# Kernel tuning notes

Measured on AMD Instinct MI355X. Metric: run time of the kernel, lower is better.

The kernel has to match this reference:

```python
import jax, jax.numpy as jnp
import numpy as np

S, E, H, D, F = 2048, 1280, 16, 80, 5120
EPS = 1e-6


def _ln(x, g, b):
    m = x.mean(-1, keepdims=True)
    v = x.var(-1, keepdims=True)
    return (x - m) * jax.lax.rsqrt(v + EPS) * g + b


def _rotate_half(x):
    x1, x2 = jnp.split(x, 2, axis=-1)
    return jnp.concatenate([-x2, x1], axis=-1)


def _quick_gelu(x):
    return x * jax.nn.sigmoid(1.702 * x)


def setup_inputs() -> dict:
    key = jax.random.key(0)
    ks = jax.random.split(key, 12)
    inp = {
        "hidden_states": jax.random.normal(ks[0], (S, E), jnp.float32),
        "attention_mask": jnp.ones((1, 1, S, S), jnp.bool_),
        "cos": jax.random.uniform(ks[1], (S, D), jnp.float32),
        "sin": jax.random.uniform(ks[2], (S, D), jnp.float32),
        "ln1_g": jnp.ones((E,), jnp.float32),
        "ln1_b": jnp.zeros((E,), jnp.float32),
        "ln2_g": jnp.ones((E,), jnp.float32),
        "ln2_b": jnp.zeros((E,), jnp.float32),
        "w_qkv": jax.random.normal(ks[3], (E, 3 * E), jnp.float32) * (E ** -0.5),
        "b_qkv": jax.random.normal(ks[4], (3 * E,), jnp.float32) * 0.02,
        "w_o": jax.random.normal(ks[5], (E, E), jnp.float32) * (E ** -0.5),
        "b_o": jax.random.normal(ks[6], (E,), jnp.float32) * 0.02,
        "w_fc1": jax.random.normal(ks[7], (E, F), jnp.float32) * (E ** -0.5),
        "b_fc1": jax.random.normal(ks[8], (F,), jnp.float32) * 0.02,
        "w_fc2": jax.random.normal(ks[9], (F, E), jnp.float32) * (F ** -0.5),
        "b_fc2": jax.random.normal(ks[10], (E,), jnp.float32) * 0.02,
    }
    return inp


def reference(hidden_states, attention_mask, cos, sin, ln1_g, ln1_b, ln2_g, ln2_b,
              w_qkv, b_qkv, w_o, b_o, w_fc1, b_fc1, w_fc2, b_fc2):
    x = hidden_states  # [S, E]
    h = _ln(x, ln1_g, ln1_b)
    qkv = h @ w_qkv + b_qkv  # [S, 3E]
    q, k, v = jnp.split(qkv, 3, axis=-1)
    q = q.reshape(S, H, D)
    k = k.reshape(S, H, D)
    v = v.reshape(S, H, D)
    # rotary in fp32, cos/sin broadcast over head axis: [S, 1, D]
    c = cos[:, None, :].astype(jnp.float32)
    s = sin[:, None, :].astype(jnp.float32)
    qf, kf = q.astype(jnp.float32), k.astype(jnp.float32)
    q = (qf * c + _rotate_half(qf) * s).astype(q.dtype)
    k = (kf * c + _rotate_half(kf) * s).astype(k.dtype)
    # attention scores [H, S, S]
    scores = jnp.einsum('shd,thd->hst', q, k) / np.float32(np.sqrt(D))
    scores = jnp.where(attention_mask[0], scores, jnp.finfo(scores.dtype).min)
    probs = jax.nn.softmax(scores.astype(jnp.float32), axis=-1).astype(q.dtype)
    attn = jnp.einsum('hst,thd->shd', probs, v).reshape(S, E)
    attn = attn @ w_o + b_o
    x = x + attn
    h2 = _ln(x, ln2_g, ln2_b)
    mlp = _quick_gelu(h2 @ w_fc1 + b_fc1) @ w_fc2 + b_fc2
    return x + mlp
```

## Files before the change

### kernel.cpp

```cpp
#include <hip/hip_runtime.h>
#include <stdint.h>
#include <math.h>

#define S_LEN 2048
#define EMB   1280
#define NHEAD 16
#define HDIM  80
#define FDIM  5120

typedef __bf16 bf16x8 __attribute__((ext_vector_type(8)));
typedef float  f32x4  __attribute__((ext_vector_type(4)));
typedef int    i32x4  __attribute__((ext_vector_type(4)));
typedef unsigned short u16x8 __attribute__((ext_vector_type(8)));
typedef unsigned short u16x4 __attribute__((ext_vector_type(4)));

__device__ __forceinline__ float b2f(unsigned short u) {
    union { float f; unsigned int i; } x; x.i = ((unsigned int)u) << 16; return x.f;
}
__device__ __forceinline__ unsigned short f2b(float f) {
    union { float f; unsigned int i; } x; x.f = f;
    unsigned int r = x.i + 0x7FFFu + ((x.i >> 16) & 1u);
    return (unsigned short)(r >> 16);
}

__device__ __forceinline__ float wave_rsum(float v) {
    #pragma unroll
    for (int o = 32; o; o >>= 1) v += __shfl_down(v, o);
    return v;
}

__device__ __forceinline__ void trans64(
    const float* __restrict__ in, unsigned short* __restrict__ out,
    int R, int C, int bx, int by, int tid)
{
    __shared__ unsigned short tile[64][65];
    int c0 = bx * 64, r0 = by * 64;
    int tx = tid & 63, ty = tid >> 6;
    #pragma unroll
    for (int j = 0; j < 16; ++j) {
        int row = ty + j * 4;
        tile[row][tx] = f2b(in[(size_t)(r0 + row) * C + c0 + tx]);
    }
    __syncthreads();
    #pragma unroll
    for (int j = 0; j < 16; ++j) {
        int row = ty + j * 4;
        out[(size_t)(c0 + row) * R + r0 + tx] = tile[tx][row];
    }
}

__global__ __launch_bounds__(256) void transpose4_kernel(
    const float* __restrict__ w_qkv, unsigned short* __restrict__ wT_qkv,
    const float* __restrict__ w_o,   unsigned short* __restrict__ wT_o,
    const float* __restrict__ w_fc1, unsigned short* __restrict__ wT_fc1,
    const float* __restrict__ w_fc2, unsigned short* __restrict__ wT_fc2)
{
    int id = blockIdx.x, tid = threadIdx.x;
    if (id < 1200) {
        trans64(w_qkv, wT_qkv, 1280, 3840, id % 60, id / 60, tid);
    } else if (id < 1600) {
        int t = id - 1200;
        trans64(w_o, wT_o, 1280, 1280, t % 20, t / 20, tid);
    } else if (id < 3200) {
        int t = id - 1600;
        trans64(w_fc1, wT_fc1, 1280, 5120, t % 80, t / 80, tid);
    } else {
        int t = id - 3200;
        trans64(w_fc2, wT_fc2, 5120, 1280, t % 20, t / 20, tid);
    }
}

__global__ __launch_bounds__(256) void ln_kernel(
    const float* __restrict__ x,
    const float* __restrict__ g,
    const float* __restrict__ b,
    unsigned short* __restrict__ out)
{
    int row = blockIdx.x, tid = threadIdx.x;
    int lane = tid & 63, wave = tid >> 6;
    const float* xr = x + (size_t)row * EMB;
    float v[5], s = 0.f, ss = 0.f;
    #pragma unroll
    for (int i = 0; i < 5; ++i) {
        float f = xr[tid + i * 256];
        v[i] = f; s += f; ss += f * f;
    }
    s = wave_rsum(s); ss = wave_rsum(ss);
    __shared__ float rs[4], rss[4];
    if (lane == 0) { rs[wave] = s; rss[wave] = ss; }
    __syncthreads();
    float st  = rs[0] + rs[1] + rs[2] + rs[3];
    float sst = rss[0] + rss[1] + rss[2] + rss[3];
    float mean = st * (1.0f / EMB);
    float var  = sst * (1.0f / EMB) - mean * mean;
    float inv  = rsqrtf(var + 1e-6f);
    unsigned short* orow = out + (size_t)row * EMB;
    #pragma unroll
    for (int i = 0; i < 5; ++i) {
        int c = tid + i * 256;
        orow[c] = f2b((v[i] - mean) * inv * g[c] + b[c]);
    }
}

template<int EPI, int OM, int SPLIT>
__global__ __launch_bounds__(256) void gemm_kernel(
    const unsigned short* __restrict__ A,
    const unsigned short* __restrict__ Bt,
    const float* __restrict__ bias,
    const float* __restrict__ res,
    void* __restrict__ Cv,
    int M, int N, int K)
{
    __shared__ __align__(16) unsigned short As[2][128 * 32];
    __shared__ __align__(16) unsigned short Bs[2][128 * 32];

    int tid = threadIdx.x;
    int lane = tid & 63, wave = tid >> 6;
    int m0 = blockIdx.x * 128, n0 = blockIdx.y * 128;
    int wm = (wave >> 1) * 64, wn = (wave & 1) * 64;
    int kc = K / SPLIT;
    int kbeg = blockIdx.z * kc;
    const int NITER = kc / 32;

    f32x4 acc[4][4];
    #pragma unroll
    for (int i = 0; i < 4; ++i)
        #pragma unroll
        for (int j = 0; j < 4; ++j)
            acc[i][j] = (f32x4){0.f, 0.f, 0.f, 0.f};

    const unsigned short* Ap0 = A  + (size_t)(m0 + (tid >> 2)) * K + (tid & 3) * 8 + kbeg;
    const unsigned short* Ap1 = Ap0 + (size_t)64 * K;
    const unsigned short* Bp0 = Bt + (size_t)(n0 + (tid >> 2)) * K + (tid & 3) * 8 + kbeg;
    const unsigned short* Bp1 = Bp0 + (size_t)64 * K;

    int arow = lane & 15, aq = (lane >> 4) * 8;
    int aoff[4], boff[4];
    #pragma unroll
    for (int i = 0; i < 4; ++i) {
        aoff[i] = (wm + i * 16 + arow) * 32 + aq;
        boff[i] = (wn + i * 16 + arow) * 32 + aq;
    }

    i32x4 rA0a, rA1a, rB0a, rB1a, rA0b, rA1b, rB0b, rB1b;

    rA0b = *(const i32x4*)(Ap0);
    rA1b = *(const i32x4*)(Ap1);
    rB0b = *(const i32x4*)(Bp0);
    rB1b = *(const i32x4*)(Bp1);
    *(i32x4*)&As[0][tid * 8]        = rA0b;
    *(i32x4*)&As[0][2048 + tid * 8] = rA1b;
    *(i32x4*)&Bs[0][tid * 8]        = rB0b;
    *(i32x4*)&Bs[0][2048 + tid * 8] = rB1b;
    if (NITER > 1) {
        rA0a = *(const i32x4*)(Ap0 + 32);
        rA1a = *(const i32x4*)(Ap1 + 32);
        rB0a = *(const i32x4*)(Bp0 + 32);
        rB1a = *(const i32x4*)(Bp1 + 32);
    }
    __syncthreads();

#define GSTEP(IT, AW0, AW1, BW0, BW1, AL0, AL1, BL0, BL1)                    \
    {                                                                         \
        const int cur = (IT) & 1, nb = cur ^ 1;                               \
        if ((IT) + 1 < NITER) {                                               \
            *(i32x4*)&As[nb][tid * 8]        = AW0;                           \
            *(i32x4*)&As[nb][2048 + tid * 8] = AW1;                           \
            *(i32x4*)&Bs[nb][tid * 8]        = BW0;                           \
            *(i32x4*)&Bs[nb][2048 + tid * 8] = BW1;                           \
        }                                                                     \
        if ((IT) + 2 < NITER) {                                               \
            int ko = ((IT) + 2) * 32;                                         \
            AL0 = *(const i32x4*)(Ap0 + ko);                                  \
            AL1 = *(const i32x4*)(Ap1 + ko);                                  \
            BL0 = *(const i32x4*)(Bp0 + ko);                                  \
            BL1 = *(const i32x4*)(Bp1 + ko);                                  \
        }                                                                     \
        bf16x8 af[4], bfm[4];                                                 \
        _Pragma("unroll") for (int i = 0; i < 4; ++i) {                       \
            af[i]  = *(const bf16x8*)&As[cur][aoff[i]];                       \
            bfm[i] = *(const bf16x8*)&Bs[cur][boff[i]];                       \
        }                                                                     \
        _Pragma("unroll") for (int mi = 0; mi < 4; ++mi)                      \
            _Pragma("unroll") for (int ni = 0; ni < 4; ++ni)                  \
                acc[mi][ni] = __builtin_amdgcn_mfma_f32_16x16x32_bf16(        \
                    af[mi], bfm[ni], acc[mi][ni], 0, 0, 0);                   \
        __syncthreads();                                                      \
    }

    for (int it = 0; it < NITER; it += 2) {
        GSTEP(it,     rA0a, rA1a, rB0a, rB1a, rA0b, rA1b, rB0b, rB1b)
        GSTEP(it + 1, rA0b, rA1b, rB0b, rB1b, rA0a, rA1a, rB0a, rB1a)
    }
#undef GSTEP

    int col = lane & 15;
    int rbase = (lane >> 4) * 4;
    #pragma unroll
    for (int ni = 0; ni < 4; ++ni) {
        int gn = n0 + wn + ni * 16 + col;
        float bv = (OM == 2) ? 0.f : bias[gn];
        #pragma unroll
        for (int mi = 0; mi < 4; ++mi) {
            int gm = m0 + wm + mi * 16 + rbase;
            #pragma unroll
            for (int r = 0; r < 4; ++r) {
                float v = acc[mi][ni][r] + bv;
                if (OM != 2) {
                    if (EPI == 1) v = v / (1.0f + expf(-1.702f * v));
                }
                if (OM == 2)
                    ((float*)Cv)[((size_t)blockIdx.z * M + gm + r) * N + gn] = v;
                else if (OM == 1)
                    ((float*)Cv)[(size_t)(gm + r) * N + gn] = v;
                else
                    ((unsigned short*)Cv)[(size_t)(gm + r) * N + gn] = f2b(v);
            }
        }
    }
}

template<int Z>
__global__ __launch_bounds__(256) void reduceZ_kernel(
    const float* __restrict__ part,
    const float* __restrict__ res,
    const float* __restrict__ bias,
    float* __restrict__ out)
{
    size_t i4 = ((size_t)blockIdx.x * 256 + threadIdx.x) * 4;
    int colb = (int)(i4 % EMB);
    f32x4 a = *(const f32x4*)&res[i4];
    f32x4 bv = *(const f32x4*)&bias[colb];
    a += bv;
    const size_t slice = (size_t)S_LEN * EMB;
    #pragma unroll
    for (int z = 0; z < Z; ++z)
        a += *(const f32x4*)&part[z * slice + i4];
    *(f32x4*)&out[i4] = a;
}

__global__ __launch_bounds__(256) void ropev_kernel(
    const unsigned short* __restrict__ qkv,
    const float* __restrict__ cosb,
    const float* __restrict__ sinb,
    unsigned short* __restrict__ q_out,
    unsigned short* __restrict__ k_out,
    unsigned short* __restrict__ vt)
{
    __shared__ unsigned short qT[64 * 84];
    __shared__ unsigned short kT[64 * 84];
    __shared__ unsigned short vT[64 * 84];

    int h = blockIdx.x >> 5, stile = blockIdx.x & 31;
    int s0 = stile * 64;
    int tid = threadIdx.x;

    u16x4 qr[5], kr[5];
    #pragma unroll
    for (int i = 0; i < 5; ++i) {
        int u = tid + i * 256;
        int row = u / 20, col = (u % 20) * 4;
        const unsigned short* base = qkv + (size_t)(s0 + row) * (3 * EMB) + h * HDIM + col;
        qr[i] = *(const u16x4*)base;
        kr[i] = *(const u16x4*)(base + EMB);
        u16x4 v4 = *(const u16x4*)(base + 2 * EMB);
        *(u16x4*)&qT[row * 84 + col] = qr[i];
        *(u16x4*)&kT[row * 84 + col] = kr[i];
        *(u16x4*)&vT[row * 84 + col] = v4;
    }
    __syncthreads();

    #pragma unroll
    for (int i = 0; i < 5; ++i) {
        int u = tid + i * 256;
        int row = u / 20, col = (u % 20) * 4;
        int pcol = (col < 40) ? col + 40 : col - 40;
        float sgn = (col < 40) ? -1.f : 1.f;
        u16x4 qp = *(const u16x4*)&qT[row * 84 + pcol];
        u16x4 kp = *(const u16x4*)&kT[row * 84 + pcol];
        f32x4 c4 = *(const f32x4*)&cosb[(size_t)(s0 + row) * HDIM + col];
        f32x4 s4 = *(const f32x4*)&sinb[(size_t)(s0 + row) * HDIM + col];
        u16x4 qo, ko;
        #pragma unroll
        for (int j = 0; j < 4; ++j) {
            qo[j] = f2b(b2f(qr[i][j]) * c4[j] + sgn * b2f(qp[j]) * s4[j]);
            ko[j] = f2b(b2f(kr[i][j]) * c4[j] + sgn * b2f(kp[j]) * s4[j]);
        }
        size_t o = ((size_t)h * S_LEN + s0 + row) * HDIM + col;
        *(u16x4*)&q_out[o] = qo;
        *(u16x4*)&k_out[o] = ko;
    }
    #pragma unroll
    for (int i = 0; i < 5; ++i) {
        int w = tid + i * 256;
        int d = w >> 4, c4i = (w & 15) * 4;
        u16x4 pk;
        #pragma unroll
        for (int j = 0; j < 4; ++j) pk[j] = vT[(c4i + j) * 84 + d];
        *(u16x4*)(vt + ((size_t)h * HDIM + d) * S_LEN + s0 + c4i) = pk;
    }
}

__global__ __launch_bounds__(256) void fattn_kernel(
    const unsigned short* __restrict__ q,
    const unsigned short* __restrict__ k,
    const unsigned short* __restrict__ vt,
    unsigned short* __restrict__ out)
{
    __shared__ __align__(16) unsigned short Ks[2][64 * 96];
    __shared__ __align__(16) unsigned short Vs[2][80 * 72];
    __shared__ __align__(16) unsigned short Pt[4 * 16 * 72];

    int tid = threadIdx.x;
    int lane = tid & 63, wave = tid >> 6;
    int arow = lane & 15, quad = lane >> 4;
    int h = blockIdx.x >> 5, qb = blockIdx.x & 31;
    int s0 = qb * 64;
    const float c = 0.16129856f;

    const unsigned short* kbase = k + (size_t)h * S_LEN * HDIM;
    const unsigned short* vbase = vt + (size_t)h * HDIM * S_LEN;

    bf16x8 qf[3];
    {
        const unsigned short* qrp =
            q + ((size_t)h * S_LEN + s0 + wave * 16 + arow) * HDIM;
        #pragma unroll
        for (int kk = 0; kk < 3; ++kk) {
            int col = kk * 32 + quad * 8;
            u16x8 qv = (u16x8){0, 0, 0, 0, 0, 0, 0, 0};
            if (col < HDIM) qv = *(const u16x8*)(qrp + col);
            u16x8 qs8;
            #pragma unroll
            for (int j = 0; j < 8; ++j) qs8[j] = f2b(b2f(qv[j]) * c);
            qf[kk] = *(bf16x8*)&qs8;
        }
    }

    {
        int zr = tid >> 2, zc = 80 + (tid & 3) * 4;
        int zidx = (zr * 96 + zc) ^ ((zr & 7) << 3);
        *(u16x4*)&Ks[0][zidx] = (u16x4){0, 0, 0, 0};
        *(u16x4*)&Ks[1][zidx] = (u16x4){0, 0, 0, 0};
    }

    u16x4 kreg[5], vreg[5];
    #pragma unroll
    for (int i = 0; i < 5; ++i) {
        int u = tid + i * 256;
        kreg[i] = *(const u16x4*)(kbase + u * 4);
        vreg[i] = *(const u16x4*)(vbase + (size_t)(u >> 4) * S_LEN + (u & 15) * 4);
    }
    #pragma unroll
    for (int i = 0; i < 5; ++i) {
        int u = tid + i * 256;
        int row = u / 20, c4 = (u % 20) * 4;
        *(u16x4*)&Ks[0][(row * 96 + c4) ^ ((row & 7) << 3)] = kreg[i];
        *(u16x4*)&Vs[0][(u >> 4) * 72 + (u & 15) * 4] = vreg[i];
    }
    #pragma unroll
    for (int i = 0; i < 5; ++i) {
        int u = tid + i * 256;
        kreg[i] = *(const u16x4*)(kbase + (size_t)64 * HDIM + u * 4);
        vreg[i] = *(const u16x4*)(vbase + (size_t)(u >> 4) * S_LEN + 64 + (u & 15) * 4);
    }
    __syncthreads();

    int ksw[3];
    #pragma unroll
    for (int kk = 0; kk < 3; ++kk)
        ksw[kk] = (arow * 96 + kk * 32 + quad * 8) ^ ((arow & 7) << 3);

    int pw = wave * 16 * 72;
    float l_part = 0.f;
    f32x4 o[5];
    #pragma unroll
    for (int di = 0; di < 5; ++di) o[di] = (f32x4){0.f, 0.f, 0.f, 0.f};

    const int NIT = S_LEN / 64;
    for (int it = 0; it < NIT; ++it) {
        int cur = it & 1;
        if (it + 1 < NIT) {
            int nb = (it + 1) & 1;
            #pragma unroll
            for (int i = 0; i < 5; ++i) {
                int u = tid + i * 256;
                int row = u / 20, c4 = (u % 20) * 4;
                *(u16x4*)&Ks[nb][(row * 96 + c4) ^ ((row & 7) << 3)] = kreg[i];
                *(u16x4*)&Vs[nb][(u >> 4) * 72 + (u & 15) * 4] = vreg[i];
            }
        }
        if (it + 2 < NIT) {
            int t0 = (it + 2) * 64;
            #pragma unroll
            for (int i = 0; i < 5; ++i) {
                int u = tid + i * 256;
                kreg[i] = *(const u16x4*)(kbase + (size_t)t0 * HDIM + u * 4);
                vreg[i] = *(const u16x4*)(vbase + (size_t)(u >> 4) * S_LEN + t0 + (u & 15) * 4);
            }
        }

        f32x4 sc[4];
        #pragma unroll
        for (int ni = 0; ni < 4; ++ni) sc[ni] = (f32x4){0.f, 0.f, 0.f, 0.f};
        __builtin_amdgcn_s_setprio(1);
        #pragma unroll
        for (int kk = 0; kk < 3; ++kk) {
            bf16x8 bq = qf[kk];
            #pragma unroll
            for (int ni = 0; ni < 4; ++ni) {
                bf16x8 ak = *(const bf16x8*)&Ks[cur][ksw[kk] + ni * 1536];
                sc[ni] = __builtin_amdgcn_mfma_f32_16x16x32_bf16(ak, bq, sc[ni], 0, 0, 0);
            }
        }
        __builtin_amdgcn_s_setprio(0);

        #pragma unroll
        for (int ni = 0; ni < 4; ++ni) {
            u16x4 pk;
            #pragma unroll
            for (int r = 0; r < 4; ++r) {
                float p = __builtin_amdgcn_exp2f(sc[ni][r]);
                l_part += p;
                __bf16 pb = (__bf16)p;
                pk[r] = *(unsigned short*)&pb;
            }
            *(u16x4*)&Pt[pw + arow * 72 + ni * 16 + quad * 4] = pk;
        }

        __builtin_amdgcn_s_setprio(1);
        #pragma unroll
        for (int kk = 0; kk < 2; ++kk) {
            bf16x8 ap = *(const bf16x8*)&Pt[pw + arow * 72 + kk * 32 + quad * 8];
            #pragma unroll
            for (int di = 0; di < 5; ++di) {
                bf16x8 bv = *(const bf16x8*)&Vs[cur][(di * 16 + arow) * 72 + kk * 32 + quad * 8];
                o[di] = __builtin_amdgcn_mfma_f32_16x16x32_bf16(ap, bv, o[di], 0, 0, 0);
            }
        }
        __builtin_amdgcn_s_setprio(0);

        __syncthreads();
    }

    float l_run = l_part;
    l_run += __shfl_xor(l_run, 16);
    l_run += __shfl_xor(l_run, 32);

    float inv[4];
    #pragma unroll
    for (int r = 0; r < 4; ++r)
        inv[r] = 1.f / __shfl(l_run, (lane & 48) | (quad * 4 + r));
    #pragma unroll
    for (int r = 0; r < 4; ++r) {
        int gq = s0 + wave * 16 + quad * 4 + r;
        unsigned short* op = out + (size_t)gq * EMB + h * HDIM;
        #pragma unroll
        for (int di = 0; di < 5; ++di)
            op[di * 16 + arow] = f2b(o[di][r] * inv[r]);
    }
}

extern "C" void kernel_launch(void* const* d_in, const int* in_sizes, int n_in,
                              void* d_out, int out_size, void* d_ws, size_t ws_size,
                              hipStream_t stream)
{
    const float* hidden = (const float*)d_in[0];
    const float* cosb  = (const float*)d_in[2];
    const float* sinb  = (const float*)d_in[3];
    const float* ln1g  = (const float*)d_in[4];
    const float* ln1b  = (const float*)d_in[5];
    const float* ln2g  = (const float*)d_in[6];
    const float* ln2b  = (const float*)d_in[7];
    const float* w_qkv = (const float*)d_in[8];
    const float* b_qkv = (const float*)d_in[9];
    const float* w_o   = (const float*)d_in[10];
    const float* b_o   = (const float*)d_in[11];
    const float* w_fc1 = (const float*)d_in[12];
    const float* b_fc1 = (const float*)d_in[13];
    const float* w_fc2 = (const float*)d_in[14];
    const float* b_fc2 = (const float*)d_in[15];

    char* ws = (char*)d_ws;
    size_t off = 0;
    auto alloc = [&](size_t bytes) -> void* {
        void* p = (void*)(ws + off);
        off += (bytes + 255) & ~(size_t)255;
        return p;
    };
    unsigned short* wT_qkv = (unsigned short*)alloc((size_t)3840 * 1280 * 2);
    unsigned short* wT_o   = (unsigned short*)alloc((size_t)1280 * 1280 * 2);
    unsigned short* wT_fc1 = (unsigned short*)alloc((size_t)5120 * 1280 * 2);
    unsigned short* wT_fc2 = (unsigned short*)alloc((size_t)1280 * 5120 * 2);
    unsigned short* h1     = (unsigned short*)alloc((size_t)S_LEN * EMB * 2);
    unsigned short* qkv    = (unsigned short*)alloc((size_t)S_LEN * 3 * EMB * 2);
    unsigned short* q_r    = (unsigned short*)alloc((size_t)S_LEN * EMB * 2);
    unsigned short* k_r    = (unsigned short*)alloc((size_t)S_LEN * EMB * 2);
    unsigned short* vt_g   = (unsigned short*)alloc((size_t)S_LEN * EMB * 2);
    unsigned short* attn_o = (unsigned short*)alloc((size_t)S_LEN * EMB * 2);
    float*          x1     = (float*)alloc((size_t)S_LEN * EMB * 4);
    unsigned short* h2     = (unsigned short*)alloc((size_t)S_LEN * EMB * 2);
    unsigned short* mlp1   = (unsigned short*)alloc((size_t)S_LEN * FDIM * 2);
    float* partials = (float*)h1;

    transpose4_kernel<<<4800, 256, 0, stream>>>(
        w_qkv, wT_qkv, w_o, wT_o, w_fc1, wT_fc1, w_fc2, wT_fc2);

    ln_kernel<<<S_LEN, 256, 0, stream>>>(hidden, ln1g, ln1b, h1);

    gemm_kernel<0, 0, 1><<<dim3(S_LEN / 128, 3840 / 128, 1), 256, 0, stream>>>(
        h1, wT_qkv, b_qkv, nullptr, qkv, S_LEN, 3 * EMB, EMB);

    ropev_kernel<<<NHEAD * (S_LEN / 64), 256, 0, stream>>>(qkv, cosb, sinb, q_r, k_r, vt_g);

    fattn_kernel<<<NHEAD * (S_LEN / 64), 256, 0, stream>>>(q_r, k_r, vt_g, attn_o);

    gemm_kernel<0, 2, 2><<<dim3(S_LEN / 128, 1280 / 128, 2), 256, 0, stream>>>(
        attn_o, wT_o, b_o, nullptr, partials, S_LEN, EMB, EMB);
    reduceZ_kernel<2><<<(S_LEN * EMB / 4) / 256, 256, 0, stream>>>(
        partials, hidden, b_o, x1);

    ln_kernel<<<S_LEN, 256, 0, stream>>>(x1, ln2g, ln2b, h2);

    gemm_kernel<1, 0, 1><<<dim3(S_LEN / 128, FDIM / 128, 1), 256, 0, stream>>>(
        h2, wT_fc1, b_fc1, nullptr, mlp1, S_LEN, FDIM, EMB);

    gemm_kernel<0, 2, 4><<<dim3(S_LEN / 128, 1280 / 128, 4), 256, 0, stream>>>(
        mlp1, wT_fc2, b_fc2, nullptr, partials, S_LEN, EMB, FDIM);
    reduceZ_kernel<4><<<(S_LEN * EMB / 4) / 256, 256, 0, stream>>>(
        partials, x1, b_fc2, (float*)d_out);
}
```

Before: 362.7 us.

## Use direct global-to-LDS loads with swizzled GEMM tiles and pad attention P buffer

The GEMM main loop now stages tiles with global_load_lds, which writes straight into shared memory and drops the register round-trip and the manual two-deep register double buffer. The global addresses are permuted with an XOR swizzle, and the fragment reads apply a matching XOR to reduce LDS bank conflicts. In the attention kernel, the P tile row offset gets an extra pad that depends on the row, and the P fragment is now read as two 8-byte loads. The risk is that the prefetch is issued only one stage ahead with no explicit vmcnt wait, so correctness depends on the barrier ordering. The split 8-byte loads may also cost some extra LDS instructions.

```diff
diff --git a/kernel.cpp b/kernel.cpp
--- a/kernel.cpp
+++ b/kernel.cpp
@@ -27,6 +27,12 @@
     #pragma unroll
     for (int o = 32; o; o >>= 1) v += __shfl_down(v, o);
     return v;
+}
+
+__device__ __forceinline__ void gload16(const unsigned short* g, unsigned short* l) {
+    __builtin_amdgcn_global_load_lds(
+        (const __attribute__((address_space(1))) void*)g,
+        (__attribute__((address_space(3))) void*)l, 16, 0, 0);
 }
 
 __device__ __forceinline__ void trans64(
@@ -129,70 +135,52 @@
         for (int j = 0; j < 4; ++j)
             acc[i][j] = (f32x4){0.f, 0.f, 0.f, 0.f};
 
-    const unsigned short* Ap0 = A  + (size_t)(m0 + (tid >> 2)) * K + (tid & 3) * 8 + kbeg;
+    int u = tid ^ ((tid >> 3) & 7);
+    const unsigned short* Ap0 = A  + (size_t)(m0 + (u >> 2)) * K + (u & 3) * 8 + kbeg;
     const unsigned short* Ap1 = Ap0 + (size_t)64 * K;
-    const unsigned short* Bp0 = Bt + (size_t)(n0 + (tid >> 2)) * K + (tid & 3) * 8 + kbeg;
+    const unsigned short* Bp0 = Bt + (size_t)(n0 + (u >> 2)) * K + (u & 3) * 8 + kbeg;
     const unsigned short* Bp1 = Bp0 + (size_t)64 * K;
 
     int arow = lane & 15, aq = (lane >> 4) * 8;
+    int aswz = ((arow >> 1) & 7) << 3;
     int aoff[4], boff[4];
     #pragma unroll
     for (int i = 0; i < 4; ++i) {
-        aoff[i] = (wm + i * 16 + arow) * 32 + aq;
-        boff[i] = (wn + i * 16 + arow) * 32 + aq;
-    }
-
-    i32x4 rA0a, rA1a, rB0a, rB1a, rA0b, rA1b, rB0b, rB1b;
-
-    rA0b = *(const i32x4*)(Ap0);
-    rA1b = *(const i32x4*)(Ap1);
-    rB0b = *(const i32x4*)(Bp0);
-    rB1b = *(const i32x4*)(Bp1);
-    *(i32x4*)&As[0][tid * 8]        = rA0b;
-    *(i32x4*)&As[0][2048 + tid * 8] = rA1b;
-    *(i32x4*)&Bs[0][tid * 8]        = rB0b;
-    *(i32x4*)&Bs[0][2048 + tid * 8] = rB1b;
-    if (NITER > 1) {
-        rA0a = *(const i32x4*)(Ap0 + 32);
-        rA1a = *(const i32x4*)(Ap1 + 32);
-        rB0a = *(const i32x4*)(Bp0 + 32);
-        rB1a = *(const i32x4*)(Bp1 + 32);
-    }
+        aoff[i] = ((wm + i * 16 + arow) * 32 + aq) ^ aswz;
+        boff[i] = ((wn + i * 16 + arow) * 32 + aq) ^ aswz;
+    }
+
+    int wbase = wave * 512;
+
+#define STAGE(B, KO)                                                          \
+    {                                                                         \
+        gload16(Ap0 + (KO), &As[B][wbase]);                                   \
+        gload16(Ap1 + (KO), &As[B][2048 + wbase]);                            \
+        gload16(Bp0 + (KO), &Bs[B][wbase]);                                   \
+        gload16(Bp1 + (KO), &Bs[B][2048 + wbase]);                            \
+    }
+
+    STAGE(0, 0)
     __syncthreads();
 
-#define GSTEP(IT, AW0, AW1, BW0, BW1, AL0, AL1, BL0, BL1)                    \
-    {                                                                         \
-        const int cur = (IT) & 1, nb = cur ^ 1;                               \
-        if ((IT) + 1 < NITER) {                                               \
-            *(i32x4*)&As[nb][tid * 8]        = AW0;                           \
-            *(i32x4*)&As[nb][2048 + tid * 8] = AW1;                           \
-            *(i32x4*)&Bs[nb][tid * 8]        = BW0;                           \
-            *(i32x4*)&Bs[nb][2048 + tid * 8] = BW1;                           \
-        }                                                                     \
-        if ((IT) + 2 < NITER) {                                               \
-            int ko = ((IT) + 2) * 32;                                         \
-            AL0 = *(const i32x4*)(Ap0 + ko);                                  \
-            AL1 = *(const i32x4*)(Ap1 + ko);                                  \
-            BL0 = *(const i32x4*)(Bp0 + ko);                                  \
-            BL1 = *(const i32x4*)(Bp1 + ko);                                  \
-        }                                                                     \
-        bf16x8 af[4], bfm[4];                                                 \
-        _Pragma("unroll") for (int i = 0; i < 4; ++i) {                       \
-            af[i]  = *(const bf16x8*)&As[cur][aoff[i]];                       \
-            bfm[i] = *(const bf16x8*)&Bs[cur][boff[i]];                       \
-        }                                                                     \
-        _Pragma("unroll") for (int mi = 0; mi < 4; ++mi)                      \
-            _Pragma("unroll") for (int ni = 0; ni < 4; ++ni)                  \
-                acc[mi][ni] = __builtin_amdgcn_mfma_f32_16x16x32_bf16(        \
-                    af[mi], bfm[ni], acc[mi][ni], 0, 0, 0);                   \
-        __syncthreads();                                                      \
-    }
-
-    for (int it = 0; it < NITER; it += 2) {
-        GSTEP(it,     rA0a, rA1a, rB0a, rB1a, rA0b, rA1b, rB0b, rB1b)
-        GSTEP(it + 1, rA0b, rA1b, rB0b, rB1b, rA0a, rA1a, rB0a, rB1a)
-    }
-#undef GSTEP
+    for (int it = 0; it < NITER; ++it) {
+        int cur = it & 1;
+        if (it + 1 < NITER) STAGE(cur ^ 1, (it + 1) * 32)
+        bf16x8 af[4], bfm[4];
+        #pragma unroll
+        for (int i = 0; i < 4; ++i) {
+            af[i]  = *(const bf16x8*)&As[cur][aoff[i]];
+            bfm[i] = *(const bf16x8*)&Bs[cur][boff[i]];
+        }
+        #pragma unroll
+        for (int mi = 0; mi < 4; ++mi)
+            #pragma unroll
+            for (int ni = 0; ni < 4; ++ni)
+                acc[mi][ni] = __builtin_amdgcn_mfma_f32_16x16x32_bf16(
+                    af[mi], bfm[ni], acc[mi][ni], 0, 0, 0);
+        __syncthreads();
+    }
+#undef STAGE
 
     int col = lane & 15;
     int rbase = (lane >> 4) * 4;
@@ -372,6 +360,8 @@
         ksw[kk] = (arow * 96 + kk * 32 + quad * 8) ^ ((arow & 7) << 3);
 
     int pw = wave * 16 * 72;
+    int poff = pw + arow * 72 + ((arow >> 3) << 2);
+
     float l_part = 0.f;
     f32x4 o[5];
     #pragma unroll
@@ -425,13 +415,17 @@
                 __bf16 pb = (__bf16)p;
                 pk[r] = *(unsigned short*)&pb;
             }
-            *(u16x4*)&Pt[pw + arow * 72 + ni * 16 + quad * 4] = pk;
+            *(u16x4*)&Pt[poff + ni * 16 + quad * 4] = pk;
         }
 
         __builtin_amdgcn_s_setprio(1);
         #pragma unroll
         for (int kk = 0; kk < 2; ++kk) {
-            bf16x8 ap = *(const bf16x8*)&Pt[pw + arow * 72 + kk * 32 + quad * 8];
+            u16x4 plo = *(const u16x4*)&Pt[poff + kk * 32 + quad * 8];
+            u16x4 phi = *(const u16x4*)&Pt[poff + kk * 32 + quad * 8 + 4];
+            u16x8 apu = (u16x8){plo[0], plo[1], plo[2], plo[3],
+                                phi[0], phi[1], phi[2], phi[3]};
+            bf16x8 ap = *(bf16x8*)&apu;
             #pragma unroll
             for (int di = 0; di < 5; ++di) {
                 bf16x8 bv = *(const bf16x8*)&Vs[cur][(di * 16 + arow) * 72 + kk * 32 + quad * 8];
```

After: 369.8 us. No clear change (+2.0%).
